# Kernel optimization log

Measured on AMD Instinct MI355X. Metric: run time of the kernel, lower is better.

Reference implementation:

```python
import jax, jax.numpy as jnp
import numpy as np

HIDDEN = 256
HEADS = 8
HEAD_DIM = HIDDEN // HEADS
RBF_DIM = 50
EPS = 1e-5


def setup_inputs() -> dict:
    key = jax.random.key(0)
    ks = jax.random.split(key, 16)
    L, P = 1024, 2048
    s = 0.02
    inp = {
        "lig_h": jax.random.normal(ks[0], (L, HIDDEN), jnp.float32),
        "prot_h": jax.random.normal(ks[1], (P, HIDDEN), jnp.float32),
        "rbf": jax.random.uniform(ks[2], (L, P, RBF_DIM), jnp.float32),
        "L": L,
        "P": P,
        "Wq": jax.random.normal(ks[3], (HIDDEN, HIDDEN), jnp.float32) * s,
        "bq": jnp.zeros((HIDDEN,), jnp.float32),
        "Wk": jax.random.normal(ks[4], (HIDDEN, HIDDEN), jnp.float32) * s,
        "bk": jnp.zeros((HIDDEN,), jnp.float32),
        "Wv": jax.random.normal(ks[5], (HIDDEN, HIDDEN), jnp.float32) * s,
        "bv": jnp.zeros((HIDDEN,), jnp.float32),
        "Wrbf": jax.random.normal(ks[6], (RBF_DIM, HEADS), jnp.float32) * s,
        "brbf": jnp.zeros((HEADS,), jnp.float32),
        "Wo": jax.random.normal(ks[7], (HIDDEN, HIDDEN), jnp.float32) * s,
        "bo": jnp.zeros((HIDDEN,), jnp.float32),
        "gamma": jnp.ones((HIDDEN,), jnp.float32),
        "beta": jnp.zeros((HIDDEN,), jnp.float32),
    }
    return inp


def reference(lig_h, prot_h, rbf, L, P, Wq, bq, Wk, bk, Wv, bv, Wrbf, brbf, Wo, bo, gamma, beta):
    scale = float(HEAD_DIM) ** 0.5
    Q = (lig_h @ Wq + bq).reshape(L, HEADS, HEAD_DIM)
    K = (prot_h @ Wk + bk).reshape(P, HEADS, HEAD_DIM)
    V = (prot_h @ Wv + bv).reshape(P, HEADS, HEAD_DIM)
    attn = jnp.einsum('lhd,phd->lph', Q, K) / scale
    dist_bias = rbf @ Wrbf + brbf          # [L, P, H]
    attn = attn + dist_bias
    attn_weights = jax.nn.softmax(attn, axis=1)  # over P (protein) axis
    attended = jnp.einsum('lph,phd->lhd', attn_weights, V).reshape(L, HIDDEN)
    y = lig_h + attended @ Wo + bo
    mu = jnp.mean(y, axis=-1, keepdims=True)
    var = jnp.var(y, axis=-1, keepdims=True)
    lig_h_out = (y - mu) * jax.lax.rsqrt(var + EPS) * gamma + beta
    return (lig_h_out, attn_weights)
```

## Files before the change

kernel.cpp:

```cpp
#include <hip/hip_runtime.h>
#include <hip/hip_bf16.h>

#define L_SZ 1024
#define P_SZ 2048
#define HID 256
#define NH 8
#define HD 32
#define NRBF 50
#define CH 16
#define NCH 128

typedef unsigned int uint32;
typedef _Float16 half2_t __attribute__((ext_vector_type(2)));
typedef __fp16 fp16x2_t __attribute__((ext_vector_type(2)));

__constant__ float kINV_SCALE = 0.17677669529663687f;

static __device__ __forceinline__ unsigned short f2h(float f) {
    union { _Float16 h; unsigned short u; } x; x.h = (_Float16)f; return x.u;
}
static __device__ __forceinline__ float h2f(unsigned short u) {
    union { unsigned short u; _Float16 h; } x; x.u = u; return (float)x.h;
}
static __device__ __forceinline__ half2_t u2h2(uint32 u) {
    union { uint32 u; half2_t h; } x; x.u = u; return x.h;
}
static __device__ __forceinline__ uint32 h22u(half2_t h) {
    union { half2_t h; uint32 u; } x; x.h = h; return x.u;
}
static __device__ __forceinline__ half2_t pk2h(float a, float b) {
    union { fp16x2_t p; half2_t h; } x; x.p = __builtin_amdgcn_cvt_pkrtz(a, b); return x.h;
}

static __device__ __forceinline__ void g2l16(const void* g, void* l) {
    __builtin_amdgcn_global_load_lds(
        (__attribute__((address_space(1))) void*)(void*)g,
        (__attribute__((address_space(3))) void*)l, 16, 0, 0);
}
static __device__ __forceinline__ void g2l4(const void* g, void* l) {
    __builtin_amdgcn_global_load_lds(
        (__attribute__((address_space(1))) void*)(void*)g,
        (__attribute__((address_space(3))) void*)l, 4, 0, 0);
}

#define WAITV0 asm volatile("s_waitcnt vmcnt(0)" ::: "memory")
#define WAITV1 asm volatile("s_waitcnt vmcnt(1)" ::: "memory")
#define CFENCE asm volatile("" ::: "memory")

__global__ __launch_bounds__(64) void k_proj(
    const float* __restrict__ lig, const float* __restrict__ prot,
    const float* __restrict__ Wq, const float* __restrict__ bq,
    const float* __restrict__ Wk, const float* __restrict__ bk,
    const float* __restrict__ Wv, const float* __restrict__ bv,
    float* __restrict__ Qf, unsigned short* __restrict__ Kb,
    unsigned short* __restrict__ Vb)
{
    __shared__ float As[8 * HID];
    const int t = threadIdx.x;
    const int r0 = blockIdx.x * 8;

    const float* src; const float* W; const float* bias; int mode; int row0;
    if (r0 < L_SZ)            { src = lig  + (size_t)r0 * HID;               W = Wq; bias = bq; mode = 0; row0 = r0; }
    else if (r0 < L_SZ + P_SZ){ src = prot + (size_t)(r0 - L_SZ) * HID;      W = Wk; bias = bk; mode = 1; row0 = r0 - L_SZ; }
    else                      { src = prot + (size_t)(r0 - L_SZ - P_SZ)*HID; W = Wv; bias = bv; mode = 2; row0 = r0 - L_SZ - P_SZ; }

    float4* A4 = (float4*)As;
    const float4* S4 = (const float4*)src;
    #pragma unroll
    for (int j = 0; j < 8; ++j) A4[t + j * 64] = S4[t + j * 64];
    __syncthreads();

    float acc[8][4];
    #pragma unroll
    for (int r = 0; r < 8; ++r)
        #pragma unroll
        for (int c = 0; c < 4; ++c) acc[r][c] = 0.f;

    for (int k4 = 0; k4 < 64; ++k4) {
        float4 av[8];
        #pragma unroll
        for (int r = 0; r < 8; ++r) av[r] = A4[r * 64 + k4];
        #pragma unroll
        for (int kk = 0; kk < 4; ++kk) {
            const float* wr = W + (size_t)(k4 * 4 + kk) * HID + t;
            #pragma unroll
            for (int c = 0; c < 4; ++c) {
                float wv = wr[c * 64];
                #pragma unroll
                for (int r = 0; r < 8; ++r)
                    acc[r][c] += ((const float*)&av[r])[kk] * wv;
            }
        }
    }

    #pragma unroll
    for (int c = 0; c < 4; ++c) {
        const int col = t + c * 64;
        const float bb = bias[col];
        #pragma unroll
        for (int r = 0; r < 8; ++r) {
            float v = acc[r][c] + bb;
            size_t idx = (size_t)(row0 + r) * HID + col;
            if (mode == 0)      Qf[idx] = v;
            else if (mode == 1) Kb[idx] = f2h(v);
            else                Vb[idx] = f2h(v);
        }
    }
}

__global__ __launch_bounds__(256, 4) void k_bias(
    const float* __restrict__ rbf, const float* __restrict__ Wrbf,
    const float* __restrict__ brbf, unsigned short* __restrict__ dbias)
{
    __shared__ __align__(16) char sm[7232];
    uint32* wtab = (uint32*)(sm + 6400);

    const int t = threadIdx.x;
    const int lane = t & 63;
    const int wv = t >> 6;
    const size_t g0 = (size_t)blockIdx.x * 32;
    const char* gb = (const char*)rbf + g0 * 200;

    g2l16(gb + wv * 1024 + (lane << 4), sm + wv * 1024);
    if (wv == 0)      g2l16(gb + 4096 + (lane << 4), sm + 4096);
    else if (wv == 1) g2l16(gb + 5120 + (lane << 4), sm + 5120);
    else if (wv == 2) g2l4 (gb + 6144 + (lane << 2), sm + 6144);

    if (t < 200) {
        int j = t >> 3, h = t & 7;
        wtab[h * 25 + j] = h22u(pk2h(Wrbf[(2 * j) * NH + h], Wrbf[(2 * j + 1) * NH + h]));
    }
    const int h = t & 7;
    const int r = t >> 3;
    float b = brbf[h];

    WAITV0;
    __syncthreads();

    half2_t wrb[25];
    #pragma unroll
    for (int j = 0; j < 25; ++j) wrb[j] = u2h2(wtab[h * 25 + j]);

    const char* rrow = sm + r * 200;
    #pragma unroll
    for (int j = 0; j < 25; ++j) {
        float2 v = *(const float2*)(rrow + j * 8);
        b = __builtin_amdgcn_fdot2(pk2h(v.x, v.y), wrb[j], b, false);
    }
    dbias[g0 * 8 + t] = f2h(b);
}

__global__ __launch_bounds__(256, 4) void k_attn(
    const float* __restrict__ Qf,
    const unsigned short* __restrict__ Kb, const unsigned short* __restrict__ Vb,
    const unsigned short* __restrict__ dbias,
    float* __restrict__ attn_out, float* __restrict__ att_ws)
{
    __shared__ __align__(16) char sm[32832];
    float* red = (float*)(sm + 32768);

    const int t = threadIdx.x;
    const int lane = t & 63;
    const int wv = t >> 6;
    const int hsub = lane >> 5;
    const int rr = (lane >> 1) & 15;
    const int half = lane & 1;
    const int hx = wv * 2 + hsub;
    const int l = blockIdx.x;
    char* aoB = (char*)attn_out + (size_t)l * (P_SZ * NH * 4);

    auto stageKV = [&](const unsigned short* src, int c, char* dst) {
        const char* gb = (const char*)src + (size_t)c * (CH * 512);
        #pragma unroll
        for (int k = 0; k < 2; ++k) {
            int s = wv * 2 + k;
            int row = s * 2 + (lane >> 5);
            int off = ((lane & 31) ^ (row & 7)) << 4;
            g2l16(gb + row * 512 + off, dst + s * 1024);
        }
    };

    half2_t qp[8];
    {
        const float* qq = Qf + (size_t)l * HID + hx * HD + half * 16;
        #pragma unroll
        for (int n = 0; n < 8; ++n) qp[n] = pk2h(qq[2 * n], qq[2 * n + 1]);
    }

    stageKV(Kb, 0, sm);
    stageKV(Vb, 0, sm + 16384);

    float mx = -3.0e38f, sme = 0.f;
    float O[16];
    #pragma unroll
    for (int d = 0; d < 16; ++d) O[d] = 0.f;

    for (int c = 0; c < NCH; ++c) {
        if (c == 0) { WAITV0; } else { WAITV1; }
        __builtin_amdgcn_s_barrier();
        CFENCE;
        const int cb = c & 1;
        const char* kb = sm + cb * 8192;
        const char* vb = sm + 16384 + cb * 8192;
        unsigned short dbu = dbias[((size_t)l * P_SZ + c * CH + rr) * 8 + hx];
        if (c + 1 < NCH) {
            stageKV(Kb, c + 1, sm + (cb ^ 1) * 8192);
            stageKV(Vb, c + 1, sm + 16384 + (cb ^ 1) * 8192);
        }
        float qk = 0.f;
        {
            const char* krow = kb + rr * 512;
            #pragma unroll
            for (int q = 0; q < 2; ++q) {
                int bc = hx * 64 + half * 32 + q * 16;
                uint4 kk = *(const uint4*)(krow + (((bc >> 4) ^ (rr & 7)) << 4));
                qk = __builtin_amdgcn_fdot2(u2h2(kk.x), qp[q * 4 + 0], qk, false);
                qk = __builtin_amdgcn_fdot2(u2h2(kk.y), qp[q * 4 + 1], qk, false);
                qk = __builtin_amdgcn_fdot2(u2h2(kk.z), qp[q * 4 + 2], qk, false);
                qk = __builtin_amdgcn_fdot2(u2h2(kk.w), qp[q * 4 + 3], qk, false);
            }
        }
        qk += __shfl_xor(qk, 1);
        float lg = qk * kINV_SCALE + h2f(dbu);

        if (lg > mx + 8.0f) {
            float ee = __expf(mx - lg);
            sme *= ee;
            #pragma unroll
            for (int d = 0; d < 16; ++d) O[d] *= ee;
            mx = lg;
        }
        float w = __expf(lg - mx);
        sme += w;

        {
            const char* vrow = vb + rr * 512;
            #pragma unroll
            for (int q = 0; q < 2; ++q) {
                int bc = hx * 64 + half * 32 + q * 16;
                uint4 vv = *(const uint4*)(vrow + (((bc >> 4) ^ (rr & 7)) << 4));
                half2_t x0 = u2h2(vv.x), x1 = u2h2(vv.y), x2 = u2h2(vv.z), x3 = u2h2(vv.w);
                O[q * 8 + 0] += w * (float)x0.x; O[q * 8 + 1] += w * (float)x0.y;
                O[q * 8 + 2] += w * (float)x1.x; O[q * 8 + 3] += w * (float)x1.y;
                O[q * 8 + 4] += w * (float)x2.x; O[q * 8 + 5] += w * (float)x2.y;
                O[q * 8 + 6] += w * (float)x3.x; O[q * 8 + 7] += w * (float)x3.y;
            }
        }
        *(unsigned short*)(aoB + (c * CH + rr) * 16 + hx * 2) = f2h(lg);
    }
    WAITV0;

    float mg = mx;
    #pragma unroll
    for (int msk = 1; msk <= 16; msk <<= 1) mg = fmaxf(mg, __shfl_xor(mg, msk));
    float e = __expf(mx - mg);
    sme *= e;
    #pragma unroll
    for (int msk = 1; msk <= 16; msk <<= 1) sme += __shfl_xor(sme, msk);
    const float invt = 2.0f / sme;

    #pragma unroll
    for (int d = 0; d < 16; ++d) O[d] *= e;
    #pragma unroll
    for (int msk = 2; msk <= 16; msk <<= 1) {
        #pragma unroll
        for (int d = 0; d < 16; ++d) O[d] += __shfl_xor(O[d], msk);
    }
    if (rr == 0) {
        float* dst = att_ws + (size_t)l * HID + hx * HD + half * 16;
        #pragma unroll
        for (int n = 0; n < 4; ++n)
            *(float4*)(dst + n * 4) = make_float4(O[n*4+0]*invt, O[n*4+1]*invt,
                                                  O[n*4+2]*invt, O[n*4+3]*invt);
        if (half == 0) { red[hx * 2] = mg; red[hx * 2 + 1] = invt; }
    }
    __syncthreads();

    {
        const int hA = 2 * (t & 3);
        const float mA = red[hA * 2],     iA = red[hA * 2 + 1];
        const float mB = red[hA * 2 + 2], iB = red[hA * 2 + 3];
        for (int n = 31; n >= 0; --n) {
            int j = t + n * 256;
            uint32 a = *(const uint32*)(aoB + 4 * j);
            float w0 = __expf(h2f((unsigned short)(a & 0xffffu)) - mA) * iA;
            float w1 = __expf(h2f((unsigned short)(a >> 16))     - mB) * iB;
            __syncthreads();
            *(float2*)(aoB + 8 * (size_t)j) = make_float2(w0, w1);
        }
    }
}

__global__ __launch_bounds__(256) void k_out(
    const float* __restrict__ att, const float* __restrict__ lig,
    const float* __restrict__ Wo, const float* __restrict__ bo,
    const float* __restrict__ gamma, const float* __restrict__ beta,
    float* __restrict__ out)
{
    __shared__ float a[HID];
    __shared__ float red[8];
    const int l = blockIdx.x, t = threadIdx.x;
    if (t < 64) ((float4*)a)[t] = ((const float4*)(att + (size_t)l * HID))[t];
    __syncthreads();

    float acc = bo[t];
    for (int k4 = 0; k4 < 64; ++k4) {
        float4 av = ((float4*)a)[k4];
        const float* wr = Wo + (size_t)(k4 * 4) * HID + t;
        acc += av.x * wr[0];
        acc += av.y * wr[HID];
        acc += av.z * wr[2 * HID];
        acc += av.w * wr[3 * HID];
    }
    float y = lig[(size_t)l * HID + t] + acc;

    float s = y, sq = y * y;
    #pragma unroll
    for (int msk = 1; msk < 64; msk <<= 1) {
        s  += __shfl_xor(s, msk);
        sq += __shfl_xor(sq, msk);
    }
    const int lane = t & 63, wvi = t >> 6;
    if (lane == 0) { red[wvi * 2] = s; red[wvi * 2 + 1] = sq; }
    __syncthreads();
    float ts = red[0] + red[2] + red[4] + red[6];
    float tq = red[1] + red[3] + red[5] + red[7];
    float mu = ts * (1.0f / HID);
    float var = tq * (1.0f / HID) - mu * mu;
    out[(size_t)l * HID + t] = (y - mu) * rsqrtf(var + 1e-5f) * gamma[t] + beta[t];
}

extern "C" void kernel_launch(void* const* d_in, const int* in_sizes, int n_in,
                              void* d_out, int out_size, void* d_ws, size_t ws_size,
                              hipStream_t stream)
{
    (void)in_sizes; (void)n_in; (void)out_size; (void)ws_size;

    const float* lig   = (const float*)d_in[0];
    const float* prot  = (const float*)d_in[1];
    const float* rbf   = (const float*)d_in[2];
    const float* Wq    = (const float*)d_in[5];
    const float* bq    = (const float*)d_in[6];
    const float* Wk    = (const float*)d_in[7];
    const float* bk    = (const float*)d_in[8];
    const float* Wv    = (const float*)d_in[9];
    const float* bv    = (const float*)d_in[10];
    const float* Wrbf  = (const float*)d_in[11];
    const float* brbf  = (const float*)d_in[12];
    const float* Wo    = (const float*)d_in[13];
    const float* bo    = (const float*)d_in[14];
    const float* gamma = (const float*)d_in[15];
    const float* beta  = (const float*)d_in[16];

    float* out0 = (float*)d_out;
    float* attn = (float*)d_out + (size_t)L_SZ * HID;

    char* ws = (char*)d_ws;
    float*          Qf     = (float*)ws;
    unsigned short* Kb     = (unsigned short*)(ws + (1u << 20));
    unsigned short* Vb     = (unsigned short*)(ws + (2u << 20));
    float*          att_ws = (float*)(ws + (3u << 20));
    unsigned short* dbias  = (unsigned short*)(ws + (4u << 20));

    hipLaunchKernelGGL(k_proj, dim3((L_SZ + 2 * P_SZ) / 8), dim3(64), 0, stream,
                       lig, prot, Wq, bq, Wk, bk, Wv, bv, Qf, Kb, Vb);
    hipLaunchKernelGGL(k_bias, dim3((L_SZ * P_SZ) / 32), dim3(256), 0, stream,
                       rbf, Wrbf, brbf, dbias);
    hipLaunchKernelGGL(k_attn, dim3(L_SZ), dim3(256), 0, stream,
                       Qf, Kb, Vb, dbias, attn, att_ws);
    hipLaunchKernelGGL(k_out, dim3(L_SZ), dim3(256), 0, stream,
                       att_ws, lig, Wo, bo, gamma, beta, out0);
}
```

Baseline: 307.7 us.

## Read K/V directly from global per-thread rows instead of LDS double-buffering

The attention kernel drops the LDS double-buffered staging of K/V chunks with barriers. Each lane now owns one protein row per iteration and loads its full 32-dim head slice of K and V straight from global (cached) memory, with no cross-lane shuffle for the dot product. The final output reduction across rows now goes through an LDS transpose instead of shuffles. This removes the per-chunk barriers and LDS traffic but doubles the accumulator registers to 32 floats and relies on L2/L1 for K/V reuse across blocks. The k_bias launch-bounds occupancy hint is also removed.

```diff
diff --git a/kernel.cpp b/kernel.cpp
--- a/kernel.cpp
+++ b/kernel.cpp
@@ -7,8 +7,6 @@
 #define NH 8
 #define HD 32
 #define NRBF 50
-#define CH 16
-#define NCH 128
 
 typedef unsigned int uint32;
 typedef _Float16 half2_t __attribute__((ext_vector_type(2)));
@@ -44,8 +42,6 @@
 }
 
 #define WAITV0 asm volatile("s_waitcnt vmcnt(0)" ::: "memory")
-#define WAITV1 asm volatile("s_waitcnt vmcnt(1)" ::: "memory")
-#define CFENCE asm volatile("" ::: "memory")
 
 __global__ __launch_bounds__(64) void k_proj(
     const float* __restrict__ lig, const float* __restrict__ prot,
@@ -108,7 +104,7 @@
     }
 }
 
-__global__ __launch_bounds__(256, 4) void k_bias(
+__global__ __launch_bounds__(256) void k_bias(
     const float* __restrict__ rbf, const float* __restrict__ Wrbf,
     const float* __restrict__ brbf, unsigned short* __restrict__ dbias)
 {
@@ -163,90 +159,90 @@
     const int lane = t & 63;
     const int wv = t >> 6;
     const int hsub = lane >> 5;
-    const int rr = (lane >> 1) & 15;
-    const int half = lane & 1;
-    const int hx = wv * 2 + hsub;
+    const int r = lane & 31;
+    const int h = wv * 2 + hsub;
     const int l = blockIdx.x;
     char* aoB = (char*)attn_out + (size_t)l * (P_SZ * NH * 4);
 
-    auto stageKV = [&](const unsigned short* src, int c, char* dst) {
-        const char* gb = (const char*)src + (size_t)c * (CH * 512);
-        #pragma unroll
-        for (int k = 0; k < 2; ++k) {
-            int s = wv * 2 + k;
-            int row = s * 2 + (lane >> 5);
-            int off = ((lane & 31) ^ (row & 7)) << 4;
-            g2l16(gb + row * 512 + off, dst + s * 1024);
-        }
-    };
-
-    half2_t qp[8];
+    half2_t qp[16];
     {
-        const float* qq = Qf + (size_t)l * HID + hx * HD + half * 16;
-        #pragma unroll
-        for (int n = 0; n < 8; ++n) qp[n] = pk2h(qq[2 * n], qq[2 * n + 1]);
-    }
-
-    stageKV(Kb, 0, sm);
-    stageKV(Vb, 0, sm + 16384);
+        const float* qq = Qf + (size_t)l * HID + h * HD;
+        #pragma unroll
+        for (int n = 0; n < 16; ++n) qp[n] = pk2h(qq[2 * n], qq[2 * n + 1]);
+    }
+
+    const char* kbase = (const char*)Kb + (size_t)r * 512 + h * 64;
+    const char* vbase = (const char*)Vb + (size_t)r * 512 + h * 64;
+    const unsigned short* db = dbias + ((size_t)l * P_SZ + r) * NH + h;
 
     float mx = -3.0e38f, sme = 0.f;
-    float O[16];
-    #pragma unroll
-    for (int d = 0; d < 16; ++d) O[d] = 0.f;
-
-    for (int c = 0; c < NCH; ++c) {
-        if (c == 0) { WAITV0; } else { WAITV1; }
-        __builtin_amdgcn_s_barrier();
-        CFENCE;
-        const int cb = c & 1;
-        const char* kb = sm + cb * 8192;
-        const char* vb = sm + 16384 + cb * 8192;
-        unsigned short dbu = dbias[((size_t)l * P_SZ + c * CH + rr) * 8 + hx];
-        if (c + 1 < NCH) {
-            stageKV(Kb, c + 1, sm + (cb ^ 1) * 8192);
-            stageKV(Vb, c + 1, sm + 16384 + (cb ^ 1) * 8192);
-        }
+    float O[32];
+    #pragma unroll
+    for (int d = 0; d < 32; ++d) O[d] = 0.f;
+
+    for (int c = 0; c < 64; ++c) {
+        const size_t roff = (size_t)c * (32 * 512);
+        unsigned short dbu = db[c * 32 * NH];
+        uint4 k0 = *(const uint4*)(kbase + roff);
+        uint4 k1 = *(const uint4*)(kbase + roff + 16);
+        uint4 k2 = *(const uint4*)(kbase + roff + 32);
+        uint4 k3 = *(const uint4*)(kbase + roff + 48);
+        uint4 v0 = *(const uint4*)(vbase + roff);
+        uint4 v1 = *(const uint4*)(vbase + roff + 16);
+        uint4 v2 = *(const uint4*)(vbase + roff + 32);
+        uint4 v3 = *(const uint4*)(vbase + roff + 48);
+
         float qk = 0.f;
-        {
-            const char* krow = kb + rr * 512;
-            #pragma unroll
-            for (int q = 0; q < 2; ++q) {
-                int bc = hx * 64 + half * 32 + q * 16;
-                uint4 kk = *(const uint4*)(krow + (((bc >> 4) ^ (rr & 7)) << 4));
-                qk = __builtin_amdgcn_fdot2(u2h2(kk.x), qp[q * 4 + 0], qk, false);
-                qk = __builtin_amdgcn_fdot2(u2h2(kk.y), qp[q * 4 + 1], qk, false);
-                qk = __builtin_amdgcn_fdot2(u2h2(kk.z), qp[q * 4 + 2], qk, false);
-                qk = __builtin_amdgcn_fdot2(u2h2(kk.w), qp[q * 4 + 3], qk, false);
-            }
-        }
-        qk += __shfl_xor(qk, 1);
+        qk = __builtin_amdgcn_fdot2(u2h2(k0.x), qp[0],  qk, false);
+        qk = __builtin_amdgcn_fdot2(u2h2(k0.y), qp[1],  qk, false);
+        qk = __builtin_amdgcn_fdot2(u2h2(k0.z), qp[2],  qk, false);
+        qk = __builtin_amdgcn_fdot2(u2h2(k0.w), qp[3],  qk, false);
+        qk = __builtin_amdgcn_fdot2(u2h2(k1.x), qp[4],  qk, false);
+        qk = __builtin_amdgcn_fdot2(u2h2(k1.y), qp[5],  qk, false);
+        qk = __builtin_amdgcn_fdot2(u2h2(k1.z), qp[6],  qk, false);
+        qk = __builtin_amdgcn_fdot2(u2h2(k1.w), qp[7],  qk, false);
+        qk = __builtin_amdgcn_fdot2(u2h2(k2.x), qp[8],  qk, false);
+        qk = __builtin_amdgcn_fdot2(u2h2(k2.y), qp[9],  qk, false);
+        qk = __builtin_amdgcn_fdot2(u2h2(k2.z), qp[10], qk, false);
+        qk = __builtin_amdgcn_fdot2(u2h2(k2.w), qp[11], qk, false);
+        qk = __builtin_amdgcn_fdot2(u2h2(k3.x), qp[12], qk, false);
+        qk = __builtin_amdgcn_fdot2(u2h2(k3.y), qp[13], qk, false);
+        qk = __builtin_amdgcn_fdot2(u2h2(k3.z), qp[14], qk, false);
+        qk = __builtin_amdgcn_fdot2(u2h2(k3.w), qp[15], qk, false);
+
         float lg = qk * kINV_SCALE + h2f(dbu);
 
         if (lg > mx + 8.0f) {
             float ee = __expf(mx - lg);
             sme *= ee;
             #pragma unroll
-            for (int d = 0; d < 16; ++d) O[d] *= ee;
+            for (int d = 0; d < 32; ++d) O[d] *= ee;
             mx = lg;
         }
         float w = __expf(lg - mx);
         sme += w;
 
         {
-            const char* vrow = vb + rr * 512;
-            #pragma unroll
-            for (int q = 0; q < 2; ++q) {
-                int bc = hx * 64 + half * 32 + q * 16;
-                uint4 vv = *(const uint4*)(vrow + (((bc >> 4) ^ (rr & 7)) << 4));
-                half2_t x0 = u2h2(vv.x), x1 = u2h2(vv.y), x2 = u2h2(vv.z), x3 = u2h2(vv.w);
-                O[q * 8 + 0] += w * (float)x0.x; O[q * 8 + 1] += w * (float)x0.y;
-                O[q * 8 + 2] += w * (float)x1.x; O[q * 8 + 3] += w * (float)x1.y;
-                O[q * 8 + 4] += w * (float)x2.x; O[q * 8 + 5] += w * (float)x2.y;
-                O[q * 8 + 6] += w * (float)x3.x; O[q * 8 + 7] += w * (float)x3.y;
-            }
-        }
-        *(unsigned short*)(aoB + (c * CH + rr) * 16 + hx * 2) = f2h(lg);
+            half2_t x;
+            x = u2h2(v0.x); O[0]  += w * (float)x.x; O[1]  += w * (float)x.y;
+            x = u2h2(v0.y); O[2]  += w * (float)x.x; O[3]  += w * (float)x.y;
+            x = u2h2(v0.z); O[4]  += w * (float)x.x; O[5]  += w * (float)x.y;
+            x = u2h2(v0.w); O[6]  += w * (float)x.x; O[7]  += w * (float)x.y;
+            x = u2h2(v1.x); O[8]  += w * (float)x.x; O[9]  += w * (float)x.y;
+            x = u2h2(v1.y); O[10] += w * (float)x.x; O[11] += w * (float)x.y;
+            x = u2h2(v1.z); O[12] += w * (float)x.x; O[13] += w * (float)x.y;
+            x = u2h2(v1.w); O[14] += w * (float)x.x; O[15] += w * (float)x.y;
+            x = u2h2(v2.x); O[16] += w * (float)x.x; O[17] += w * (float)x.y;
+            x = u2h2(v2.y); O[18] += w * (float)x.x; O[19] += w * (float)x.y;
+            x = u2h2(v2.z); O[20] += w * (float)x.x; O[21] += w * (float)x.y;
+            x = u2h2(v2.w); O[22] += w * (float)x.x; O[23] += w * (float)x.y;
+            x = u2h2(v3.x); O[24] += w * (float)x.x; O[25] += w * (float)x.y;
+            x = u2h2(v3.y); O[26] += w * (float)x.x; O[27] += w * (float)x.y;
+            x = u2h2(v3.z); O[28] += w * (float)x.x; O[29] += w * (float)x.y;
+            x = u2h2(v3.w); O[30] += w * (float)x.x; O[31] += w * (float)x.y;
+        }
+
+        *(unsigned short*)(aoB + (size_t)(c * 32 + r) * 16 + h * 2) = f2h(lg);
     }
     WAITV0;
 
@@ -257,24 +253,25 @@
     sme *= e;
     #pragma unroll
     for (int msk = 1; msk <= 16; msk <<= 1) sme += __shfl_xor(sme, msk);
-    const float invt = 2.0f / sme;
-
-    #pragma unroll
-    for (int d = 0; d < 16; ++d) O[d] *= e;
-    #pragma unroll
-    for (int msk = 2; msk <= 16; msk <<= 1) {
-        #pragma unroll
-        for (int d = 0; d < 16; ++d) O[d] += __shfl_xor(O[d], msk);
-    }
-    if (rr == 0) {
-        float* dst = att_ws + (size_t)l * HID + hx * HD + half * 16;
-        #pragma unroll
-        for (int n = 0; n < 4; ++n)
-            *(float4*)(dst + n * 4) = make_float4(O[n*4+0]*invt, O[n*4+1]*invt,
-                                                  O[n*4+2]*invt, O[n*4+3]*invt);
-        if (half == 0) { red[hx * 2] = mg; red[hx * 2 + 1] = invt; }
-    }
-    __syncthreads();
+    float inv = 1.0f / sme;
+    if (r == 0) { red[h * 2] = mg; red[h * 2 + 1] = inv; }
+    const float scl = e * inv;
+
+    __syncthreads();
+
+    {
+        float* otr = (float*)sm;
+        #pragma unroll
+        for (int d = 0; d < 32; ++d)
+            otr[h * 1024 + r * 32 + ((d + r) & 31)] = O[d] * scl;
+        __syncthreads();
+        const int hh = t >> 5, dd = t & 31;
+        float a = 0.f;
+        #pragma unroll
+        for (int rr = 0; rr < 32; ++rr)
+            a += otr[hh * 1024 + rr * 32 + ((dd + rr) & 31)];
+        att_ws[(size_t)l * HID + hh * HD + dd] = a;
+    }
 
     {
         const int hA = 2 * (t & 3);
@@ -282,7 +279,7 @@
         const float mB = red[hA * 2 + 2], iB = red[hA * 2 + 3];
         for (int n = 31; n >= 0; --n) {
             int j = t + n * 256;
-            uint32 a = *(const uint32*)(aoB + 4 * j);
+            uint32 a = *(const uint32*)(aoB + 4 * (size_t)j);
             float w0 = __expf(h2f((unsigned short)(a & 0xffffu)) - mA) * iA;
             float w1 = __expf(h2f((unsigned short)(a >> 16))     - mB) * iB;
             __syncthreads();
```

New measurement: 414.6 us. 1.35x slower.

## Persistent double-buffered rbf bias kernel; stagger and prefetch chunks in attention

Applied to the files above, without the earlier changes.

The bias kernel now has each block process 32 chunks of 32 rows, with a double-buffered async global-to-LDS pipeline. The Wrbf weights are loaded once into registers instead of once per small block, which cuts launch and setup overhead and keeps the loads overlapped with compute. The attention kernel rotates its starting chunk per ligand row so that blocks spread their K/V reads across different chunks. It also prefetches the next chunk's bias value one iteration ahead to hide the global load latency. Risk: far fewer bias blocks (2048), so parallelism and occupancy depend on the new launch bound of 6.

```diff
diff --git a/kernel.cpp b/kernel.cpp
--- a/kernel.cpp
+++ b/kernel.cpp
@@ -24,9 +24,6 @@
 }
 static __device__ __forceinline__ half2_t u2h2(uint32 u) {
     union { uint32 u; half2_t h; } x; x.u = u; return x.h;
-}
-static __device__ __forceinline__ uint32 h22u(half2_t h) {
-    union { half2_t h; uint32 u; } x; x.h = h; return x.u;
 }
 static __device__ __forceinline__ half2_t pk2h(float a, float b) {
     union { fp16x2_t p; half2_t h; } x; x.p = __builtin_amdgcn_cvt_pkrtz(a, b); return x.h;
@@ -108,46 +105,49 @@
     }
 }
 
-__global__ __launch_bounds__(256, 4) void k_bias(
+__global__ __launch_bounds__(256, 6) void k_bias(
     const float* __restrict__ rbf, const float* __restrict__ Wrbf,
     const float* __restrict__ brbf, unsigned short* __restrict__ dbias)
 {
-    __shared__ __align__(16) char sm[7232];
-    uint32* wtab = (uint32*)(sm + 6400);
+    __shared__ __align__(16) char sm[12800];
 
     const int t = threadIdx.x;
     const int lane = t & 63;
     const int wv = t >> 6;
-    const size_t g0 = (size_t)blockIdx.x * 32;
-    const char* gb = (const char*)rbf + g0 * 200;
-
-    g2l16(gb + wv * 1024 + (lane << 4), sm + wv * 1024);
-    if (wv == 0)      g2l16(gb + 4096 + (lane << 4), sm + 4096);
-    else if (wv == 1) g2l16(gb + 5120 + (lane << 4), sm + 5120);
-    else if (wv == 2) g2l4 (gb + 6144 + (lane << 2), sm + 6144);
-
-    if (t < 200) {
-        int j = t >> 3, h = t & 7;
-        wtab[h * 25 + j] = h22u(pk2h(Wrbf[(2 * j) * NH + h], Wrbf[(2 * j + 1) * NH + h]));
-    }
     const int h = t & 7;
     const int r = t >> 3;
-    float b = brbf[h];
-
-    WAITV0;
-    __syncthreads();
+    const size_t c0 = (size_t)blockIdx.x * 32;
+
+    auto stage = [&](size_t ch, char* dst) {
+        const char* gb = (const char*)rbf + ch * 6400;
+        g2l16(gb + wv * 1024 + (lane << 4), dst + wv * 1024);
+        if (wv == 0)      g2l16(gb + 4096 + (lane << 4), dst + 4096);
+        else if (wv == 1) g2l16(gb + 5120 + (lane << 4), dst + 5120);
+        else if (wv == 2) g2l4 (gb + 6144 + (lane << 2), dst + 6144);
+    };
 
     half2_t wrb[25];
     #pragma unroll
-    for (int j = 0; j < 25; ++j) wrb[j] = u2h2(wtab[h * 25 + j]);
-
-    const char* rrow = sm + r * 200;
-    #pragma unroll
-    for (int j = 0; j < 25; ++j) {
-        float2 v = *(const float2*)(rrow + j * 8);
-        b = __builtin_amdgcn_fdot2(pk2h(v.x, v.y), wrb[j], b, false);
-    }
-    dbias[g0 * 8 + t] = f2h(b);
+    for (int j = 0; j < 25; ++j)
+        wrb[j] = pk2h(Wrbf[(2 * j) * NH + h], Wrbf[(2 * j + 1) * NH + h]);
+    const float bh = brbf[h];
+
+    stage(c0, sm);
+    for (int k = 0; k < 32; ++k) {
+        if (k == 0) { WAITV0; } else { WAITV1; }
+        __builtin_amdgcn_s_barrier();
+        CFENCE;
+        const int kb = k & 1;
+        if (k + 1 < 32) stage(c0 + k + 1, sm + (kb ^ 1) * 6400);
+        const char* rrow = sm + kb * 6400 + r * 200;
+        float b = bh;
+        #pragma unroll
+        for (int j = 0; j < 25; ++j) {
+            float2 v = *(const float2*)(rrow + j * 8);
+            b = __builtin_amdgcn_fdot2(pk2h(v.x, v.y), wrb[j], b, false);
+        }
+        dbias[(c0 + k) * 256 + t] = f2h(b);
+    }
 }
 
 __global__ __launch_bounds__(256, 4) void k_attn(
@@ -187,8 +187,12 @@
         for (int n = 0; n < 8; ++n) qp[n] = pk2h(qq[2 * n], qq[2 * n + 1]);
     }
 
-    stageKV(Kb, 0, sm);
-    stageKV(Vb, 0, sm + 16384);
+    const int boff = l & (NCH - 1);
+    const unsigned short* dbL = dbias + (size_t)l * (P_SZ * NH) + rr * NH + hx;
+
+    stageKV(Kb, boff, sm);
+    stageKV(Vb, boff, sm + 16384);
+    unsigned short dbu_cur = dbL[(size_t)boff * (CH * NH)];
 
     float mx = -3.0e38f, sme = 0.f;
     float O[16];
@@ -196,16 +200,19 @@
     for (int d = 0; d < 16; ++d) O[d] = 0.f;
 
     for (int c = 0; c < NCH; ++c) {
+        const int ca = (c + boff) & (NCH - 1);
         if (c == 0) { WAITV0; } else { WAITV1; }
         __builtin_amdgcn_s_barrier();
         CFENCE;
         const int cb = c & 1;
         const char* kb = sm + cb * 8192;
         const char* vb = sm + 16384 + cb * 8192;
-        unsigned short dbu = dbias[((size_t)l * P_SZ + c * CH + rr) * 8 + hx];
+        unsigned short dbu_next = 0;
         if (c + 1 < NCH) {
-            stageKV(Kb, c + 1, sm + (cb ^ 1) * 8192);
-            stageKV(Vb, c + 1, sm + 16384 + (cb ^ 1) * 8192);
+            const int can = (c + 1 + boff) & (NCH - 1);
+            stageKV(Kb, can, sm + (cb ^ 1) * 8192);
+            stageKV(Vb, can, sm + 16384 + (cb ^ 1) * 8192);
+            dbu_next = dbL[(size_t)can * (CH * NH)];
         }
         float qk = 0.f;
         {
@@ -221,7 +228,7 @@
             }
         }
         qk += __shfl_xor(qk, 1);
-        float lg = qk * kINV_SCALE + h2f(dbu);
+        float lg = qk * kINV_SCALE + h2f(dbu_cur);
 
         if (lg > mx + 8.0f) {
             float ee = __expf(mx - lg);
@@ -246,7 +253,8 @@
                 O[q * 8 + 6] += w * (float)x3.x; O[q * 8 + 7] += w * (float)x3.y;
             }
         }
-        *(unsigned short*)(aoB + (c * CH + rr) * 16 + hx * 2) = f2h(lg);
+        *(unsigned short*)(aoB + (ca * CH + rr) * 16 + hx * 2) = f2h(lg);
+        dbu_cur = dbu_next;
     }
     WAITV0;
 
@@ -282,7 +290,7 @@
         const float mB = red[hA * 2 + 2], iB = red[hA * 2 + 3];
         for (int n = 31; n >= 0; --n) {
             int j = t + n * 256;
-            uint32 a = *(const uint32*)(aoB + 4 * j);
+            uint32 a = *(const uint32*)(aoB + 4 * (size_t)j);
             float w0 = __expf(h2f((unsigned short)(a & 0xffffu)) - mA) * iA;
             float w1 = __expf(h2f((unsigned short)(a >> 16))     - mB) * iB;
             __syncthreads();
@@ -364,7 +372,7 @@
 
     hipLaunchKernelGGL(k_proj, dim3((L_SZ + 2 * P_SZ) / 8), dim3(64), 0, stream,
                        lig, prot, Wq, bq, Wk, bk, Wv, bv, Qf, Kb, Vb);
-    hipLaunchKernelGGL(k_bias, dim3((L_SZ * P_SZ) / 32), dim3(256), 0, stream,
+    hipLaunchKernelGGL(k_bias, dim3((L_SZ * P_SZ) / 32 / 32), dim3(256), 0, stream,
                        rbf, Wrbf, brbf, dbias);
     hipLaunchKernelGGL(k_attn, dim3(L_SZ), dim3(256), 0, stream,
                        Qf, Kb, Vb, dbias, attn, att_ws);
```

Measured after the change: 320.4 us. 1.04x slower.
